# Performance work log

Measured on AMD Instinct MI355X. Metric: run time of the kernel, lower is better.

Reference implementation:

```python
import jax, jax.numpy as jnp
import numpy as np

B, C, H, W, NH = 8, 256, 32, 32, 4  # batch, channels, height, width, heads


def groupnorm(x, w, b, eps=1e-5):
    # GroupNorm with 1 group: normalize over (C,H,W) per sample
    mu = x.mean(axis=(1, 2, 3), keepdims=True)
    var = x.var(axis=(1, 2, 3), keepdims=True)
    xn = (x - mu) * jax.lax.rsqrt(var + eps)
    return xn * w[None, :, None, None] + b[None, :, None, None]


def setup_inputs() -> dict:
    key = jax.random.key(0)
    ks = jax.random.split(key, 6)
    C4 = 4 * C
    s = lambda k, shape, scale: jax.random.normal(k, shape, jnp.float32) * scale
    return {
        "x": jax.random.normal(ks[0], (B, C, H, W), jnp.float32),
        "qkv_w": s(ks[1], (3 * C, C), 0.05),   # 1x1 conv, no bias
        "uh_w": s(ks[2], (C, C), 0.05),
        "uh_b": jnp.zeros((C,), jnp.float32),
        "n1_w": jnp.ones((C,), jnp.float32),
        "n1_b": jnp.zeros((C,), jnp.float32),
        "n2_w": jnp.ones((C,), jnp.float32),
        "n2_b": jnp.zeros((C,), jnp.float32),
        "f1_w": s(ks[3], (C4, C), 0.05),
        "f1_b": jnp.zeros((C4,), jnp.float32),
        "f2_w": s(ks[4], (C, C4), 0.05),
        "f2_b": jnp.zeros((C,), jnp.float32),
        # torch inits these to 0; use nonzero values so both branches contribute
        "gamma_attn": jnp.array(0.5, jnp.float32),
        "gamma_ffn": jnp.array(0.5, jnp.float32),
    }


def reference(x, qkv_w, uh_w, uh_b, n1_w, n1_b, n2_w, n2_b,
              f1_w, f1_b, f2_w, f2_b, gamma_attn, gamma_ffn):
    Bx, Cx, Hx, Wx = x.shape
    N = Hx * Wx
    dk = Cx // NH
    # --- attention branch (eval mode: DropPath is identity) ---
    xn = groupnorm(x, n1_w, n1_b).reshape(Bx, Cx, N)
    qkv = jnp.einsum('oc,bcn->bon', qkv_w, xn)          # 1x1 conv == channel matmul
    q, k, v = [t.reshape(Bx, NH, dk, N) for t in jnp.split(qkv, 3, axis=1)]
    scores = jnp.einsum('bhdi,bhdj->bhij', q, k) / np.float32(np.sqrt(dk))
    attn = jax.nn.softmax(scores, axis=-1)               # [B,H,N,N]
    out = jnp.einsum('bhij,bhdj->bhdi', attn, v).reshape(Bx, Cx, N)
    uh = jnp.einsum('oc,bcn->bon', uh_w, out) + uh_b[None, :, None]
    x2 = x + gamma_attn * uh.reshape(Bx, Cx, Hx, Wx)
    # --- FFN branch ---
    h = groupnorm(x2, n2_w, n2_b).reshape(Bx, Cx, N)
    h = jax.nn.silu(jnp.einsum('oc,bcn->bon', f1_w, h) + f1_b[None, :, None])
    h = jnp.einsum('oc,bcn->bon', f2_w, h) + f2_b[None, :, None]
    return x2 + gamma_ffn * h.reshape(Bx, Cx, Hx, Wx)
```

## Files before the change

kernel.cpp:

```cpp
#include <hip/hip_runtime.h>
#include <math.h>

#define Bsz 8
#define Cch 256
#define Nsp 1024
#define NHd 4
#define QS  0.18033688011112042f

using bf16x8  = __attribute__((ext_vector_type(8))) short;
using f32x4   = __attribute__((ext_vector_type(4))) float;
using ushort8 = __attribute__((ext_vector_type(8))) unsigned short;
#define MFMA(a,b,c) __builtin_amdgcn_mfma_f32_16x16x32_bf16(a,b,c,0,0,0)

__device__ inline unsigned short f2bf(float f) {
    unsigned int u = __float_as_uint(f);
    u = u + 0x7fffu + ((u >> 16) & 1u);
    return (unsigned short)(u >> 16);
}
__device__ inline float bf2f(unsigned short u) {
    return __uint_as_float((unsigned int)u << 16);
}
__device__ inline unsigned int cvtpk(float lo, float hi) {
    unsigned int r;
    asm("v_cvt_pk_bf16_f32 %0, %1, %2" : "=v"(r) : "v"(lo), "v"(hi));
    return r;
}

__global__ __launch_bounds__(256) void wconv_gn(const float* __restrict__ a, const float* __restrict__ b,
                                                const float* __restrict__ c, const float* __restrict__ d,
                                                unsigned short* __restrict__ o,
                                                const float* __restrict__ x,
                                                float* __restrict__ part) {
    if (blockIdx.x < 3072) {
        size_t i = (size_t)blockIdx.x * 256 + threadIdx.x;
        float v;
        if (i < 196608) v = a[i];
        else if (i < 262144) v = b[i - 196608];
        else if (i < 524288) v = c[i - 262144];
        else v = d[i - 524288];
        o[i] = f2bf(v);
        return;
    }
    int blk = blockIdx.x - 3072;
    int bb = blk >> 6;
    const float* xb = x + (size_t)bb * (Cch * Nsp) + (size_t)(blk & 63) * 4096;
    int t = threadIdx.x;
    float s = 0.f, s2 = 0.f;
    for (int i = t; i < 4096; i += 256) { float v = xb[i]; s += v; s2 += v * v; }
    __shared__ float sh[256], sh2[256];
    sh[t] = s; sh2[t] = s2; __syncthreads();
    for (int off = 128; off; off >>= 1) {
        if (t < off) { sh[t] += sh[t + off]; sh2[t] += sh2[t + off]; }
        __syncthreads();
    }
    if (t == 0) { part[blk * 2] = sh[0]; part[blk * 2 + 1] = sh2[0]; }
}

template<int K, int KL, int NFRAG>
__global__ __launch_bounds__(256, 4) void gemm_lds(
        const unsigned short* __restrict__ W,
        const unsigned short* __restrict__ Xcl,
        int epi, int act, int xmode,
        unsigned short* __restrict__ ocl, int Ocl, int ocol0,
        unsigned short* __restrict__ orm,
        float* __restrict__ pf, const float* __restrict__ res,
        unsigned short* __restrict__ x2cl,
        const float* __restrict__ gamma, const float* __restrict__ bias,
        float* __restrict__ part,
        const float* __restrict__ gnpart,
        const float* __restrict__ gnw, const float* __restrict__ gnb) {
    static_assert(KL == 256 && K == 256, "single-round K only");
    constexpr int NTILE = NFRAG * 16;
    constexpr int CPR = KL / 8;
    constexpr int TOTCH = NTILE * CPR;
    int b = blockIdx.z, nb = blockIdx.x, ob = blockIdx.y;
    int t = threadIdx.x, w = t >> 6, l = t & 63, lg = l >> 4, lm = l & 15;
    __shared__ unsigned short Xs[NTILE * KL];
    __shared__ float sgn[2];
    const unsigned short* Xb = Xcl + ((size_t)b * Nsp + nb * NTILE) * K;
    int o_base = ob * 256 + w * 64;
    const unsigned short* Wp = W + (size_t)(o_base + lm) * K + 8 * lg;
    int m8 = lm & 7;

    bf16x8 wA0, wA1, wA2, wA3, wB0, wB1, wB2, wB3, wC0, wC1, wC2, wC3;
    #define WL(d0, d1, d2, d3, ks_) do {                                   \
        d0 = *(const bf16x8*)(Wp + (size_t)(0)      + (ks_) * 32);         \
        d1 = *(const bf16x8*)(Wp + (size_t)16 * K   + (ks_) * 32);         \
        d2 = *(const bf16x8*)(Wp + (size_t)32 * K   + (ks_) * 32);         \
        d3 = *(const bf16x8*)(Wp + (size_t)48 * K   + (ks_) * 32);         \
    } while (0)
    WL(wA0, wA1, wA2, wA3, 0);
    WL(wB0, wB1, wB2, wB3, 1);

    if (xmode == 0) {
        #pragma unroll
        for (int i = 0; i < TOTCH / 256; i++) {
            int c = i * 256 + t;
            int n = c / CPR, s = c % CPR;
            int gc = s ^ (n & 7);
            *(bf16x8*)&Xs[c * 8] = *(const bf16x8*)(Xb + (size_t)n * K + gc * 8);
        }
    } else if (xmode == 1) {
        if (t < 64) {
            float s = gnpart[(b * 64 + t) * 2], s2 = gnpart[(b * 64 + t) * 2 + 1];
            for (int m = 1; m < 64; m <<= 1) { s += __shfl_xor(s, m); s2 += __shfl_xor(s2, m); }
            if (t == 0) {
                float inv_n = 1.f / (Cch * Nsp);
                float mu = s * inv_n;
                float var = s2 * inv_n - mu * mu;
                sgn[0] = mu; sgn[1] = rsqrtf(var + 1e-5f);
            }
        }
        __syncthreads();
        float mu = sgn[0], rs = sgn[1];
        #pragma unroll
        for (int i = 0; i < TOTCH / 256; i++) {
            int c = i * 256 + t;
            int n = c / CPR, s = c % CPR;
            int gc = s ^ (n & 7);
            ushort8 xv = *(const ushort8*)(Xb + (size_t)n * K + gc * 8);
            f32x4 w0 = *(const f32x4*)(gnw + gc * 8);
            f32x4 w1 = *(const f32x4*)(gnw + gc * 8 + 4);
            f32x4 b0 = *(const f32x4*)(gnb + gc * 8);
            f32x4 b1 = *(const f32x4*)(gnb + gc * 8 + 4);
            ushort8 rr;
            #pragma unroll
            for (int j = 0; j < 4; j++) {
                rr[j]     = f2bf((bf2f(xv[j])     - mu) * rs * w0[j] + b0[j]);
                rr[4 + j] = f2bf((bf2f(xv[4 + j]) - mu) * rs * w1[j] + b1[j]);
            }
            *(ushort8*)&Xs[c * 8] = rr;
        }
    } else if (xmode == 2) {
        const size_t SPO = (size_t)Bsz * Nsp * Cch;
        #pragma unroll
        for (int i = 0; i < TOTCH / 256; i++) {
            int c = i * 256 + t;
            int n = c / CPR, s = c % CPR;
            int gc = s ^ (n & 7);
            const unsigned short* p0 = Xb + (size_t)n * K + gc * 8;
            int h = gc >> 3;
            int gn = nb * NTILE + n;
            float a0[8] = {};
            float lsum = 0.f;
            #pragma unroll
            for (int sp = 0; sp < 4; sp++) {
                ushort8 ov = *(const ushort8*)(p0 + (size_t)sp * SPO);
                #pragma unroll
                for (int j = 0; j < 8; j++) a0[j] += bf2f(ov[j]);
                lsum += gnpart[(((size_t)sp * Bsz + b) * NHd + h) * Nsp + gn];
            }
            float inv = 1.f / lsum;
            ushort8 rr;
            #pragma unroll
            for (int j = 0; j < 8; j++) rr[j] = f2bf(a0[j] * inv);
            *(ushort8*)&Xs[c * 8] = rr;
        }
    } else {
        if (t < 64) {
            float s = gnpart[(b * 64 + t) * 2], s2 = gnpart[(b * 64 + t) * 2 + 1];
            for (int m = 1; m < 64; m <<= 1) { s += __shfl_xor(s, m); s2 += __shfl_xor(s2, m); }
            if (t == 0) {
                float inv_n = 1.f / (Cch * Nsp);
                float mu = s * inv_n;
                float var = s2 * inv_n - mu * mu;
                sgn[0] = mu; sgn[1] = rsqrtf(var + 1e-5f);
            }
        }
        __syncthreads();
        float mu = sgn[0], rs = sgn[1];
        int n = t & 31;
        #pragma unroll
        for (int i = 0; i < 4; i++) {
            int G = i * 8 + (t >> 5);
            const float* xr = res + ((size_t)b * Cch + G * 8) * Nsp + (size_t)nb * NTILE + n;
            ushort8 rr;
            #pragma unroll
            for (int j = 0; j < 8; j++) {
                float val = xr[(size_t)j * Nsp];
                rr[j] = f2bf((val - mu) * rs * gnw[G * 8 + j] + gnb[G * 8 + j]);
            }
            int slot = G ^ (n & 7);
            *(ushort8*)&Xs[(n * 32 + slot) * 8] = rr;
        }
    }
    __syncthreads();

    f32x4 acc[4][NFRAG] = {};
    #define KS(w0_, w1_, w2_, w3_, ks_) do {                               \
        _Pragma("unroll")                                                  \
        for (int nf = 0; nf < NFRAG; nf++) {                               \
            int slot = ((ks_) * 4 + lg) ^ m8;                              \
            bf16x8 xf = *(const bf16x8*)&Xs[((nf * 16 + lm) * CPR + slot) * 8]; \
            acc[0][nf] = MFMA(w0_, xf, acc[0][nf]);                        \
            acc[1][nf] = MFMA(w1_, xf, acc[1][nf]);                        \
            acc[2][nf] = MFMA(w2_, xf, acc[2][nf]);                        \
            acc[3][nf] = MFMA(w3_, xf, acc[3][nf]);                        \
        }                                                                  \
    } while (0)
    WL(wC0, wC1, wC2, wC3, 2); KS(wA0, wA1, wA2, wA3, 0);
    WL(wA0, wA1, wA2, wA3, 3); KS(wB0, wB1, wB2, wB3, 1);
    WL(wB0, wB1, wB2, wB3, 4); KS(wC0, wC1, wC2, wC3, 2);
    WL(wC0, wC1, wC2, wC3, 5); KS(wA0, wA1, wA2, wA3, 3);
    WL(wA0, wA1, wA2, wA3, 6); KS(wB0, wB1, wB2, wB3, 4);
    WL(wB0, wB1, wB2, wB3, 7); KS(wC0, wC1, wC2, wC3, 5);
    KS(wA0, wA1, wA2, wA3, 6);
    KS(wB0, wB1, wB2, wB3, 7);
    #undef WL
    #undef KS

    if (epi == 0) {
        if (act == 3 && o_base >= 512) {
            #pragma unroll
            for (int nf = 0; nf < NFRAG; nf++) {
                int n = nb * NTILE + nf * 16 + lm;
                #pragma unroll
                for (int q = 0; q < 4; q++)
                    #pragma unroll
                    for (int r = 0; r < 4; r++) {
                        int o = o_base + q * 16 + 4 * lg + r - 512;
                        orm[((size_t)b * Cch + o) * Nsp + n] = f2bf(acc[q][nf][r]);
                    }
            }
        } else {
            float sc = (act == 3 && o_base < 256) ? QS : 1.f;
            #pragma unroll
            for (int nf = 0; nf < NFRAG; nf++) {
                int n = nb * NTILE + nf * 16 + lm;
                unsigned short* dst = ocl + ((size_t)b * Nsp + n) * Ocl + ocol0 + o_base + 4 * lg;
                #pragma unroll
                for (int q = 0; q < 4; q++) {
                    unsigned long long pk = 0;
                    #pragma unroll
                    for (int r = 0; r < 4; r++) {
                        int o = o_base + q * 16 + 4 * lg + r;
                        float v = acc[q][nf][r];
                        if (bias) v += bias[o];
                        if (act == 1) v = v / (1.f + __expf(-v));
                        else v *= sc;
                        pk |= (unsigned long long)f2bf(v) << (16 * r);
                    }
                    *(unsigned long long*)(dst + q * 16) = pk;
                }
            }
        }
    } else {
        float g = gamma[0];
        float ps = 0.f, ps2 = 0.f;
        #pragma unroll
        for (int nf = 0; nf < NFRAG; nf++) {
            int n = nb * NTILE + nf * 16 + lm;
            unsigned short* cdst = x2cl + ((size_t)b * Nsp + n) * Cch + o_base + 4 * lg;
            #pragma unroll
            for (int q = 0; q < 4; q++) {
                unsigned long long pk = 0;
                #pragma unroll
                for (int r = 0; r < 4; r++) {
                    int o = o_base + q * 16 + 4 * lg + r;
                    float v = acc[q][nf][r];
                    if (bias) v += bias[o];
                    size_t idx = ((size_t)b * Cch + o) * Nsp + n;
                    float ov = res[idx] + g * v;
                    pf[idx] = ov;
                    ps += ov; ps2 += ov * ov;
                    pk |= (unsigned long long)f2bf(ov) << (16 * r);
                }
                *(unsigned long long*)(cdst + q * 16) = pk;
            }
        }
        float* rsh  = (float*)&Xs[0];
        float* rsh2 = rsh + 256;
        __syncthreads();
        rsh[t] = ps; rsh2[t] = ps2; __syncthreads();
        for (int off = 128; off; off >>= 1) {
            if (t < off) { rsh[t] += rsh[t + off]; rsh2[t] += rsh2[t + off]; }
            __syncthreads();
        }
        if (t == 0) {
            int slot = b * gridDim.x + nb;
            part[slot * 2] = rsh[0]; part[slot * 2 + 1] = rsh2[0];
        }
    }
}

__global__ __launch_bounds__(1024, 4) void ffn_fused(
        const unsigned short* __restrict__ Wf1,
        const unsigned short* __restrict__ Wf2,
        const unsigned short* __restrict__ x2cl,
        const float* __restrict__ gnpart,
        const float* __restrict__ gnw, const float* __restrict__ gnb,
        const float* __restrict__ f1b, const float* __restrict__ f2b,
        const float* __restrict__ gamma,
        const float* __restrict__ x2, float* __restrict__ out) {
    int b = blockIdx.z, nb = blockIdx.x;
    int t = threadIdx.x, w = t >> 6, l = t & 63, lg = l >> 4, lm = l & 15;
    __shared__ unsigned short Xs[32 * 256];
    __shared__ unsigned short H[4][32 * 256];
    __shared__ float sgn[2];
    const unsigned short* Xb = x2cl + ((size_t)b * Nsp + nb * 32) * 256;
    int m8 = lm & 7;

    bf16x8 wA0, wA1, wA2, wA3, wB0, wB1, wB2, wB3, wC0, wC1, wC2, wC3;
    const unsigned short* Wp = Wf1 + (size_t)(w * 64 + lm) * 256 + 8 * lg;
    #define WL1(d0, d1, d2, d3, ks_) do {                                  \
        d0 = *(const bf16x8*)(Wp + (ks_) * 32);                            \
        d1 = *(const bf16x8*)(Wp + (size_t)16 * 256 + (ks_) * 32);         \
        d2 = *(const bf16x8*)(Wp + (size_t)32 * 256 + (ks_) * 32);         \
        d3 = *(const bf16x8*)(Wp + (size_t)48 * 256 + (ks_) * 32);         \
    } while (0)

    if (t < 64) {
        float s = gnpart[(b * 64 + t) * 2], s2 = gnpart[(b * 64 + t) * 2 + 1];
        for (int m = 1; m < 64; m <<= 1) { s += __shfl_xor(s, m); s2 += __shfl_xor(s2, m); }
        if (t == 0) {
            float inv_n = 1.f / (Cch * Nsp);
            float mu = s * inv_n;
            float var = s2 * inv_n - mu * mu;
            sgn[0] = mu; sgn[1] = rsqrtf(var + 1e-5f);
        }
    }
    WL1(wA0, wA1, wA2, wA3, 0);
    WL1(wB0, wB1, wB2, wB3, 1);
    __syncthreads();
    {
        float mu = sgn[0], rs = sgn[1];
        int c = t;
        int n = c >> 5, s = c & 31;
        int gc = s ^ (n & 7);
        ushort8 xv = *(const ushort8*)(Xb + (size_t)n * 256 + gc * 8);
        f32x4 w0 = *(const f32x4*)(gnw + gc * 8);
        f32x4 w1 = *(const f32x4*)(gnw + gc * 8 + 4);
        f32x4 b0 = *(const f32x4*)(gnb + gc * 8);
        f32x4 b1 = *(const f32x4*)(gnb + gc * 8 + 4);
        ushort8 rr;
        #pragma unroll
        for (int j = 0; j < 4; j++) {
            rr[j]     = f2bf((bf2f(xv[j])     - mu) * rs * w0[j] + b0[j]);
            rr[4 + j] = f2bf((bf2f(xv[4 + j]) - mu) * rs * w1[j] + b1[j]);
        }
        *(ushort8*)&Xs[c * 8] = rr;
    }
    __syncthreads();

    f32x4 acc[4][2];
    #pragma unroll
    for (int q = 0; q < 4; q++)
        #pragma unroll
        for (int nf = 0; nf < 2; nf++) acc[q][nf] = (f32x4){0.f, 0.f, 0.f, 0.f};
    #define KS1(w0_, w1_, w2_, w3_, ks_) do {                              \
        _Pragma("unroll")                                                  \
        for (int nf = 0; nf < 2; nf++) {                                   \
            int slot = ((ks_) * 4 + lg) ^ m8;                              \
            bf16x8 xf = *(const bf16x8*)&Xs[((nf * 16 + lm) * 32 + slot) * 8]; \
            acc[0][nf] = MFMA(w0_, xf, acc[0][nf]);                        \
            acc[1][nf] = MFMA(w1_, xf, acc[1][nf]);                        \
            acc[2][nf] = MFMA(w2_, xf, acc[2][nf]);                        \
            acc[3][nf] = MFMA(w3_, xf, acc[3][nf]);                        \
        }                                                                  \
    } while (0)
    WL1(wC0, wC1, wC2, wC3, 2); KS1(wA0, wA1, wA2, wA3, 0);
    WL1(wA0, wA1, wA2, wA3, 3); KS1(wB0, wB1, wB2, wB3, 1);
    WL1(wB0, wB1, wB2, wB3, 4); KS1(wC0, wC1, wC2, wC3, 2);
    WL1(wC0, wC1, wC2, wC3, 5); KS1(wA0, wA1, wA2, wA3, 3);
    WL1(wA0, wA1, wA2, wA3, 6); KS1(wB0, wB1, wB2, wB3, 4);
    WL1(wB0, wB1, wB2, wB3, 7); KS1(wC0, wC1, wC2, wC3, 5);
    KS1(wA0, wA1, wA2, wA3, 6);
    KS1(wB0, wB1, wB2, wB3, 7);
    #undef WL1
    #undef KS1

    const unsigned short* Wp2 = Wf2 + (size_t)(w * 16 + lm) * 1024 + 8 * lg;
    bf16x8 fa, fb, fc, fd, fe, ff;
    #define WL2(d0, ks_) d0 = *(const bf16x8*)(Wp2 + (ks_) * 32)
    WL2(fa, 0); WL2(fb, 1); WL2(fc, 2); WL2(fd, 3);

    {
        int hb = w >> 2;
        #pragma unroll
        for (int nf = 0; nf < 2; nf++) {
            int n = nf * 16 + lm;
            #pragma unroll
            for (int q = 0; q < 4; q++) {
                unsigned long long pk = 0;
                #pragma unroll
                for (int r = 0; r < 4; r++) {
                    int o1 = w * 64 + q * 16 + 4 * lg + r;
                    float v = acc[q][nf][r] + f1b[o1];
                    v = v / (1.f + __expf(-v));
                    pk |= (unsigned long long)f2bf(v) << (16 * r);
                }
                int G = (w & 3) * 8 + q * 2 + (lg >> 1);
                int slot = G ^ (n & 7);
                *(unsigned long long*)&H[hb][(n * 32 + slot) * 8 + 4 * (lg & 1)] = pk;
            }
        }
    }
    __syncthreads();

    f32x4 ac2[2] = {};
    #define KS2(e0, g_) do {                                               \
        int slot = (((g_) & 7) * 4 + lg) ^ m8;                             \
        const unsigned short* Hp = H[(g_) >> 3];                           \
        _Pragma("unroll")                                                  \
        for (int nf = 0; nf < 2; nf++) {                                   \
            bf16x8 xf = *(const bf16x8*)&Hp[((nf * 16 + lm) * 32 + slot) * 8]; \
            ac2[nf] = MFMA(e0, xf, ac2[nf]);                               \
        }                                                                  \
    } while (0)
    WL2(fe, 4);  KS2(fa, 0);
    WL2(ff, 5);  KS2(fb, 1);
    WL2(fa, 6);  KS2(fc, 2);
    WL2(fb, 7);  KS2(fd, 3);
    WL2(fc, 8);  KS2(fe, 4);
    WL2(fd, 9);  KS2(ff, 5);
    WL2(fe, 10); KS2(fa, 6);
    WL2(ff, 11); KS2(fb, 7);
    WL2(fa, 12); KS2(fc, 8);
    WL2(fb, 13); KS2(fd, 9);
    WL2(fc, 14); KS2(fe, 10);
    WL2(fd, 15); KS2(ff, 11);
    WL2(fe, 16); KS2(fa, 12);
    WL2(ff, 17); KS2(fb, 13);
    WL2(fa, 18); KS2(fc, 14);
    WL2(fb, 19); KS2(fd, 15);
    WL2(fc, 20); KS2(fe, 16);
    WL2(fd, 21); KS2(ff, 17);
    WL2(fe, 22); KS2(fa, 18);
    WL2(ff, 23); KS2(fb, 19);
    WL2(fa, 24); KS2(fc, 20);
    WL2(fb, 25); KS2(fd, 21);
    WL2(fc, 26); KS2(fe, 22);
    WL2(fd, 27); KS2(ff, 23);
    WL2(fe, 28); KS2(fa, 24);
    WL2(ff, 29); KS2(fb, 25);
    WL2(fa, 30); KS2(fc, 26);
    WL2(fb, 31); KS2(fd, 27);
    KS2(fe, 28);
    KS2(ff, 29);
    KS2(fa, 30);
    KS2(fb, 31);
    #undef WL2
    #undef KS2

    float gm = gamma[0];
    #pragma unroll
    for (int nf = 0; nf < 2; nf++) {
        int n = nb * 32 + nf * 16 + lm;
        #pragma unroll
        for (int r = 0; r < 4; r++) {
            int o = w * 16 + 4 * lg + r;
            size_t idx = ((size_t)b * Cch + o) * Nsp + n;
            out[idx] = x2[idx] + gm * (ac2[nf][r] + f2b[o]);
        }
    }
}

__global__ __launch_bounds__(256) void attn_mfma8(const unsigned short* __restrict__ qk,
                                                  const unsigned short* __restrict__ v,
                                                  unsigned short* __restrict__ Opart,
                                                  float* __restrict__ lpart) {
    int L = blockIdx.x;
    int xcd = L & 7, jj = L >> 3;
    int g = xcd * 4 + (jj >> 5);
    int m = jj & 31;
    int h = g & 3, b = g >> 2;
    int ib = m & 7, sp = m >> 3;
    int t = threadIdx.x, w = t >> 6, l = t & 63, lg = l >> 4, lm = l & 15;
    __shared__ unsigned short KVs[2][4096];
    __shared__ unsigned short P[4][2][32][36];
    int i0 = ib * 128 + w * 32;
    int j0 = sp * 256;
    const unsigned short* qb = qk + ((size_t)b * Nsp + i0 + lm) * 512 + h * 64 + 8 * lg;
    bf16x8 qf00 = *(const bf16x8*)(qb);
    bf16x8 qf01 = *(const bf16x8*)(qb + 32);
    bf16x8 qf10 = *(const bf16x8*)(qb + 16 * 512);
    bf16x8 qf11 = *(const bf16x8*)(qb + 16 * 512 + 32);

    const unsigned short *gs0, *gs1;
    int lo0, lo1;
    size_t gstep;
    if (t < 128) {
        int c = 2 * t;
        int r = c >> 3, s = c & 7, swr = r & 7;
        const unsigned short* rowp = qk + ((size_t)b * Nsp + j0 + r) * 512 + 256 + h * 64;
        gs0 = rowp + ((s ^ swr) * 8);
        gs1 = rowp + (((s + 1) ^ swr) * 8);
        lo0 = c * 8; lo1 = lo0 + 8;
        gstep = (size_t)32 * 512;
    } else {
        int c = 2 * (t - 128);
        int d = c >> 2, s = c & 3, swd = d & 3;
        const unsigned short* rowp = v + ((size_t)b * Cch + h * 64 + d) * Nsp + j0;
        gs0 = rowp + ((s ^ swd) * 8);
        gs1 = rowp + (((s + 1) ^ swd) * 8);
        lo0 = 2048 + c * 8; lo1 = lo0 + 8;
        gstep = 32;
    }
    int cA = (lg ^ (lm & 7)) * 8;
    int cB = ((4 + lg) ^ (lm & 7)) * 8;
    int cV = (lg ^ (lm & 3)) * 8;

    f32x4 O00 = {}, O01 = {}, O02 = {}, O03 = {};
    f32x4 O10 = {}, O11 = {}, O12 = {}, O13 = {};
    float ls0 = 0.f, ls1 = 0.f;
    bf16x8 sg0, sg1;

    #define ISSUE(tile) do { sg0 = *(const bf16x8*)(gs0 + (size_t)(tile) * gstep); \
                             sg1 = *(const bf16x8*)(gs1 + (size_t)(tile) * gstep); } while (0)
    #define WRITE(bu) do { *(bf16x8*)&KVs[bu][lo0] = sg0; \
                           *(bf16x8*)&KVs[bu][lo1] = sg1; } while (0)
    #define QKC8(bu, pb) do {                                                     \
        const unsigned short* Ka = KVs[bu] + lm * 64;                             \
        const unsigned short* Kc = KVs[bu] + (16 + lm) * 64;                      \
        bf16x8 k00 = *(const bf16x8*)(Ka + cA);                                   \
        bf16x8 k01 = *(const bf16x8*)(Ka + cB);                                   \
        bf16x8 k10 = *(const bf16x8*)(Kc + cA);                                   \
        bf16x8 k11 = *(const bf16x8*)(Kc + cB);                                   \
        f32x4 s00 = {}, s01 = {}, s10 = {}, s11 = {};                             \
        s00 = MFMA(k00, qf00, s00); s00 = MFMA(k01, qf01, s00);                   \
        s01 = MFMA(k00, qf10, s01); s01 = MFMA(k01, qf11, s01);                   \
        s10 = MFMA(k10, qf00, s10); s10 = MFMA(k11, qf01, s10);                   \
        s11 = MFMA(k10, qf10, s11); s11 = MFMA(k11, qf11, s11);                   \
        float p0, p1, p2, p3; uint2 pk;                                           \
        p0 = exp2f(s00[0]); p1 = exp2f(s00[1]); p2 = exp2f(s00[2]); p3 = exp2f(s00[3]); \
        ls0 += (p0 + p1) + (p2 + p3);                                             \
        pk.x = cvtpk(p0, p1); pk.y = cvtpk(p2, p3);                               \
        *(uint2*)&P[w][pb][lm][4 * lg] = pk;                                      \
        p0 = exp2f(s01[0]); p1 = exp2f(s01[1]); p2 = exp2f(s01[2]); p3 = exp2f(s01[3]); \
        ls1 += (p0 + p1) + (p2 + p3);                                             \
        pk.x = cvtpk(p0, p1); pk.y = cvtpk(p2, p3);                               \
        *(uint2*)&P[w][pb][16 + lm][4 * lg] = pk;                                 \
        p0 = exp2f(s10[0]); p1 = exp2f(s10[1]); p2 = exp2f(s10[2]); p3 = exp2f(s10[3]); \
        ls0 += (p0 + p1) + (p2 + p3);                                             \
        pk.x = cvtpk(p0, p1); pk.y = cvtpk(p2, p3);                               \
        *(uint2*)&P[w][pb][lm][16 + 4 * lg] = pk;                                 \
        p0 = exp2f(s11[0]); p1 = exp2f(s11[1]); p2 = exp2f(s11[2]); p3 = exp2f(s11[3]); \
        ls1 += (p0 + p1) + (p2 + p3);                                             \
        pk.x = cvtpk(p0, p1); pk.y = cvtpk(p2, p3);                               \
        *(uint2*)&P[w][pb][16 + lm][16 + 4 * lg] = pk;                            \
    } while (0)
    #define PVC8(bu, pb) do {                                                     \
        bf16x8 pa0 = *(const bf16x8*)&P[w][pb][lm][8 * lg];                       \
        bf16x8 pa1 = *(const bf16x8*)&P[w][pb][16 + lm][8 * lg];                  \
        const unsigned short* Vl = KVs[bu] + 2048;                                \
        bf16x8 v0 = *(const bf16x8*)(Vl + lm * 32 + cV);                          \
        bf16x8 v1 = *(const bf16x8*)(Vl + (16 + lm) * 32 + cV);                   \
        bf16x8 v2 = *(const bf16x8*)(Vl + (32 + lm) * 32 + cV);                   \
        bf16x8 v3 = *(const bf16x8*)(Vl + (48 + lm) * 32 + cV);                   \
        O00 = MFMA(v0, pa0, O00); O10 = MFMA(v0, pa1, O10);                       \
        O01 = MFMA(v1, pa0, O01); O11 = MFMA(v1, pa1, O11);                       \
        O02 = MFMA(v2, pa0, O02); O12 = MFMA(v2, pa1, O12);                       \
        O03 = MFMA(v3, pa0, O03); O13 = MFMA(v3, pa1, O13);                       \
    } while (0)

    ISSUE(0); WRITE(0); __syncthreads();
    ISSUE(1);
    QKC8(0, 0);
    __syncthreads();
    WRITE(1);
    __syncthreads();
    #pragma unroll
    for (int tt = 1; tt < 8; tt++) {
        if (tt < 7) ISSUE(tt + 1);
        QKC8(tt & 1, tt & 1);
        PVC8((tt - 1) & 1, (tt - 1) & 1);
        __syncthreads();
        if (tt < 7) WRITE((tt + 1) & 1);
        __syncthreads();
    }
    PVC8(1, 1);
    #undef ISSUE
    #undef WRITE
    #undef QKC8
    #undef PVC8

    ls0 += __shfl_xor(ls0, 16); ls0 += __shfl_xor(ls0, 32);
    ls1 += __shfl_xor(ls1, 16); ls1 += __shfl_xor(ls1, 32);
    if (lg == 0) {
        float* lp = lpart + (((size_t)sp * Bsz + b) * NHd + h) * Nsp + i0 + lm;
        lp[0] = ls0;
        lp[16] = ls1;
    }
    unsigned short* ob0 = Opart + (((size_t)sp * Bsz + b) * Nsp + i0 + lm) * Cch + h * 64 + 4 * lg;
    unsigned short* ob1 = ob0 + (size_t)16 * Cch;
    uint2 pk;
    #define STO(dt, Oa, Ob_) \
        pk.x = cvtpk(Oa[0], Oa[1]); pk.y = cvtpk(Oa[2], Oa[3]); \
        *(uint2*)(ob0 + dt * 16) = pk; \
        pk.x = cvtpk(Ob_[0], Ob_[1]); pk.y = cvtpk(Ob_[2], Ob_[3]); \
        *(uint2*)(ob1 + dt * 16) = pk;
    STO(0, O00, O10) STO(1, O01, O11) STO(2, O02, O12) STO(3, O03, O13)
    #undef STO
}

extern "C" void kernel_launch(void* const* d_in, const int* in_sizes, int n_in,
                              void* d_out, int out_size, void* d_ws, size_t ws_size,
                              hipStream_t stream) {
    const float* x      = (const float*)d_in[0];
    const float* qkv_w  = (const float*)d_in[1];
    const float* uh_w   = (const float*)d_in[2];
    const float* uh_b   = (const float*)d_in[3];
    const float* n1_w   = (const float*)d_in[4];
    const float* n1_b   = (const float*)d_in[5];
    const float* n2_w   = (const float*)d_in[6];
    const float* n2_b   = (const float*)d_in[7];
    const float* f1_w   = (const float*)d_in[8];
    const float* f1_b   = (const float*)d_in[9];
    const float* f2_w   = (const float*)d_in[10];
    const float* f2_b   = (const float*)d_in[11];
    const float* g_attn = (const float*)d_in[12];
    const float* g_ffn  = (const float*)d_in[13];
    float* out = (float*)d_out;
    char* ws = (char*)d_ws;

    float*          part1   = (float*)(ws + 1024);
    float*          part2   = (float*)(ws + 5120);
    unsigned short* wbf     = (unsigned short*)(ws + 16384);
    float*          lpart   = (float*)(ws + 2097152);
    unsigned short* qk_cl   = (unsigned short*)(ws + 6291456);
    unsigned short* vbuf    = (unsigned short*)(ws + 14680064);
    unsigned short* x2cl    = (unsigned short*)(ws + 14680064);
    unsigned short* Opart   = (unsigned short*)(ws + 23068672);
    float*          x2      = (float*)(ws + 50331648);

    unsigned short* wbf_qkv = wbf;
    unsigned short* wbf_uh  = wbf + 196608;
    unsigned short* wbf_f1  = wbf + 262144;
    unsigned short* wbf_f2  = wbf + 524288;

    wconv_gn<<<3584, 256, 0, stream>>>(qkv_w, uh_w, f1_w, f2_w, wbf, x, part1);

    gemm_lds<256, 256, 2><<<dim3(32, 3, Bsz), 256, 0, stream>>>(wbf_qkv,
        (const unsigned short*)x, 0, 3, 3,
        qk_cl, 512, 0, vbuf, nullptr, x, nullptr, nullptr, nullptr, nullptr,
        part1, n1_w, n1_b);
    attn_mfma8<<<1024, 256, 0, stream>>>(qk_cl, vbuf, Opart, lpart);
    gemm_lds<256, 256, 1><<<dim3(64, 1, Bsz), 256, 0, stream>>>(wbf_uh, Opart, 2, 0, 2,
        nullptr, 0, 0, nullptr, x2, x, x2cl, g_attn, uh_b, part2,
        lpart, nullptr, nullptr);

    ffn_fused<<<dim3(32, 1, Bsz), 1024, 0, stream>>>(wbf_f1, wbf_f2, x2cl,
        part2, n2_w, n2_b, f1_b, f2_b, g_ffn, x2, out);
}
```

Baseline: 106.0 us.

## Split FFN second GEMM over K across warps with LDS tree reduction

Each warp in the FFN down-projection used to own 16 output channels and walk the full K=1024 range. Now it owns 64 output channels and one quarter of K. Each B-fragment read from shared memory feeds four MFMAs instead of one, which cuts LDS traffic per MFMA and reuses the register tiles from the first GEMM. The four partial sums are combined through a two-level reduction in shared memory, which adds extra barriers, LDS write and read traffic, and leaves only a quarter of the warps doing the final epilogue stores.

```diff
diff --git a/kernel.cpp b/kernel.cpp
--- a/kernel.cpp
+++ b/kernel.cpp
@@ -369,10 +369,16 @@
     #undef WL1
     #undef KS1
 
-    const unsigned short* Wp2 = Wf2 + (size_t)(w * 16 + lm) * 1024 + 8 * lg;
-    bf16x8 fa, fb, fc, fd, fe, ff;
-    #define WL2(d0, ks_) d0 = *(const bf16x8*)(Wp2 + (ks_) * 32)
-    WL2(fa, 0); WL2(fb, 1); WL2(fc, 2); WL2(fd, 3);
+    int kq = w >> 2, wo = w & 3;
+    const unsigned short* Wp2 = Wf2 + (size_t)(wo * 64 + lm) * 1024 + kq * 256 + 8 * lg;
+    #define WL2(d0, d1, d2, d3, ks_) do {                                  \
+        d0 = *(const bf16x8*)(Wp2 + (ks_) * 32);                           \
+        d1 = *(const bf16x8*)(Wp2 + (size_t)16 * 1024 + (ks_) * 32);       \
+        d2 = *(const bf16x8*)(Wp2 + (size_t)32 * 1024 + (ks_) * 32);       \
+        d3 = *(const bf16x8*)(Wp2 + (size_t)48 * 1024 + (ks_) * 32);       \
+    } while (0)
+    WL2(wA0, wA1, wA2, wA3, 0);
+    WL2(wB0, wB1, wB2, wB3, 1);
 
     {
         int hb = w >> 2;
@@ -397,60 +403,86 @@
     }
     __syncthreads();
 
-    f32x4 ac2[2] = {};
-    #define KS2(e0, g_) do {                                               \
-        int slot = (((g_) & 7) * 4 + lg) ^ m8;                             \
-        const unsigned short* Hp = H[(g_) >> 3];                           \
+    #pragma unroll
+    for (int q = 0; q < 4; q++)
+        #pragma unroll
+        for (int nf = 0; nf < 2; nf++) acc[q][nf] = (f32x4){0.f, 0.f, 0.f, 0.f};
+    const unsigned short* Hq = H[kq];
+    #define KS2(w0_, w1_, w2_, w3_, ks_) do {                              \
         _Pragma("unroll")                                                  \
         for (int nf = 0; nf < 2; nf++) {                                   \
-            bf16x8 xf = *(const bf16x8*)&Hp[((nf * 16 + lm) * 32 + slot) * 8]; \
-            ac2[nf] = MFMA(e0, xf, ac2[nf]);                               \
+            int slot = ((ks_) * 4 + lg) ^ m8;                              \
+            bf16x8 xf = *(const bf16x8*)&Hq[((nf * 16 + lm) * 32 + slot) * 8]; \
+            acc[0][nf] = MFMA(w0_, xf, acc[0][nf]);                        \
+            acc[1][nf] = MFMA(w1_, xf, acc[1][nf]);                        \
+            acc[2][nf] = MFMA(w2_, xf, acc[2][nf]);                        \
+            acc[3][nf] = MFMA(w3_, xf, acc[3][nf]);                        \
         }                                                                  \
     } while (0)
-    WL2(fe, 4);  KS2(fa, 0);
-    WL2(ff, 5);  KS2(fb, 1);
-    WL2(fa, 6);  KS2(fc, 2);
-    WL2(fb, 7);  KS2(fd, 3);
-    WL2(fc, 8);  KS2(fe, 4);
-    WL2(fd, 9);  KS2(ff, 5);
-    WL2(fe, 10); KS2(fa, 6);
-    WL2(ff, 11); KS2(fb, 7);
-    WL2(fa, 12); KS2(fc, 8);
-    WL2(fb, 13); KS2(fd, 9);
-    WL2(fc, 14); KS2(fe, 10);
-    WL2(fd, 15); KS2(ff, 11);
-    WL2(fe, 16); KS2(fa, 12);
-    WL2(ff, 17); KS2(fb, 13);
-    WL2(fa, 18); KS2(fc, 14);
-    WL2(fb, 19); KS2(fd, 15);
-    WL2(fc, 20); KS2(fe, 16);
-    WL2(fd, 21); KS2(ff, 17);
-    WL2(fe, 22); KS2(fa, 18);
-    WL2(ff, 23); KS2(fb, 19);
-    WL2(fa, 24); KS2(fc, 20);
-    WL2(fb, 25); KS2(fd, 21);
-    WL2(fc, 26); KS2(fe, 22);
-    WL2(fd, 27); KS2(ff, 23);
-    WL2(fe, 28); KS2(fa, 24);
-    WL2(ff, 29); KS2(fb, 25);
-    WL2(fa, 30); KS2(fc, 26);
-    WL2(fb, 31); KS2(fd, 27);
-    KS2(fe, 28);
-    KS2(ff, 29);
-    KS2(fa, 30);
-    KS2(fb, 31);
+    WL2(wC0, wC1, wC2, wC3, 2); KS2(wA0, wA1, wA2, wA3, 0);
+    WL2(wA0, wA1, wA2, wA3, 3); KS2(wB0, wB1, wB2, wB3, 1);
+    WL2(wB0, wB1, wB2, wB3, 4); KS2(wC0, wC1, wC2, wC3, 2);
+    WL2(wC0, wC1, wC2, wC3, 5); KS2(wA0, wA1, wA2, wA3, 3);
+    WL2(wA0, wA1, wA2, wA3, 6); KS2(wB0, wB1, wB2, wB3, 4);
+    WL2(wB0, wB1, wB2, wB3, 7); KS2(wC0, wC1, wC2, wC3, 5);
+    KS2(wA0, wA1, wA2, wA3, 6);
+    KS2(wB0, wB1, wB2, wB3, 7);
     #undef WL2
     #undef KS2
 
-    float gm = gamma[0];
-    #pragma unroll
-    for (int nf = 0; nf < 2; nf++) {
-        int n = nb * 32 + nf * 16 + lm;
-        #pragma unroll
-        for (int r = 0; r < 4; r++) {
-            int o = w * 16 + 4 * lg + r;
-            size_t idx = ((size_t)b * Cch + o) * Nsp + n;
-            out[idx] = x2[idx] + gm * (ac2[nf][r] + f2b[o]);
+    __syncthreads();
+    float* hr = (float*)H;
+    if (kq & 1) {
+        float* bp = hr + ((kq >> 1) * 4 + wo) * 2048 + l * 32;
+        #pragma unroll
+        for (int q = 0; q < 4; q++) {
+            *(f32x4*)(bp + q * 8)     = acc[q][0];
+            *(f32x4*)(bp + q * 8 + 4) = acc[q][1];
+        }
+    }
+    __syncthreads();
+    if (!(kq & 1)) {
+        float* bp = hr + ((kq >> 1) * 4 + wo) * 2048 + l * 32;
+        #pragma unroll
+        for (int q = 0; q < 4; q++) {
+            f32x4 p0 = *(const f32x4*)(bp + q * 8);
+            f32x4 p1 = *(const f32x4*)(bp + q * 8 + 4);
+            #pragma unroll
+            for (int r = 0; r < 4; r++) { acc[q][0][r] += p0[r]; acc[q][1][r] += p1[r]; }
+        }
+    }
+    __syncthreads();
+    if (kq == 2) {
+        float* bp = hr + wo * 2048 + l * 32;
+        #pragma unroll
+        for (int q = 0; q < 4; q++) {
+            *(f32x4*)(bp + q * 8)     = acc[q][0];
+            *(f32x4*)(bp + q * 8 + 4) = acc[q][1];
+        }
+    }
+    __syncthreads();
+    if (kq == 0) {
+        float* bp = hr + wo * 2048 + l * 32;
+        #pragma unroll
+        for (int q = 0; q < 4; q++) {
+            f32x4 p0 = *(const f32x4*)(bp + q * 8);
+            f32x4 p1 = *(const f32x4*)(bp + q * 8 + 4);
+            #pragma unroll
+            for (int r = 0; r < 4; r++) { acc[q][0][r] += p0[r]; acc[q][1][r] += p1[r]; }
+        }
+        float gm = gamma[0];
+        #pragma unroll
+        for (int nf = 0; nf < 2; nf++) {
+            int n = nb * 32 + nf * 16 + lm;
+            #pragma unroll
+            for (int q = 0; q < 4; q++) {
+                #pragma unroll
+                for (int r = 0; r < 4; r++) {
+                    int o = wo * 64 + q * 16 + 4 * lg + r;
+                    size_t idx = ((size_t)b * Cch + o) * Nsp + n;
+                    out[idx] = x2[idx] + gm * (acc[q][nf][r] + f2b[o]);
+                }
+            }
         }
     }
 }
```

Result: slower. 110.3 us (+4.0%).
